# Kernel optimization log

Hardware: AMD Instinct MI355X
Metric: run time of the kernel (lower is better)

## Reference

```python
import math
import jax, jax.numpy as jnp
import numpy as np

SR = 48000
FRAME_HOP = 240
F0_MIN = 20.0
F0_MAX = 5000.0
F0_BINS = 64
VEL_DIM = 8
N_HARM = 128
NOISE_FFT = 1024
N_NOISE = NOISE_FFT // 2 + 1
HOP = NOISE_FFT // 4
PAD = NOISE_FFT // 2


def lin_interp(x, size):
    # matches F.interpolate(mode='linear', align_corners=False) along last axis
    T_in = x.shape[-1]
    pos = (jnp.arange(size, dtype=jnp.float32) + 0.5) * (T_in / size) - 0.5
    pos = jnp.clip(pos, 0.0, T_in - 1.0)
    lo = jnp.floor(pos).astype(jnp.int32)
    hi = jnp.minimum(lo + 1, T_in - 1)
    fr = pos - lo.astype(jnp.float32)
    return x[..., lo] * (1.0 - fr) + x[..., hi] * fr


def encode_f0(f0):
    f0s = jnp.clip(f0, F0_MIN, None)
    fn = jnp.clip((jnp.log(f0s) - math.log(F0_MIN)) / (math.log(F0_MAX) - math.log(F0_MIN)), 0.0, 1.0)
    i = jnp.arange(1, F0_BINS // 2 + 1, dtype=jnp.float32)
    ang = math.pi * i * fn[..., None]  # (B,T,bins/2)
    enc = jnp.stack([jnp.sin(ang), jnp.cos(ang)], axis=-1).reshape(f0.shape + (F0_BINS,))
    return enc * (f0 > 0).astype(jnp.float32)[..., None]


def encode_velocity(vel):
    vn = jnp.clip(vel.astype(jnp.float32) / 7.0, 0.0, 1.0)
    i = jnp.arange(1, VEL_DIM // 2 + 1, dtype=jnp.float32)
    ang = math.pi * i * vn[..., None]
    return jnp.stack([jnp.sin(ang), jnp.cos(ang)], axis=-1).reshape(vel.shape + (VEL_DIM,))


def gru(x, W_ih, W_hh, b_ih, b_hh):
    # torch nn.GRU, 1 layer, batch_first; gate order r,z,n
    B, T, _ = x.shape
    H = W_hh.shape[1]
    gi = x @ W_ih.T + b_ih  # (B,T,3H)

    def step(h, g):
        gh = h @ W_hh.T + b_hh
        ir, iz, in_ = jnp.split(g, 3, axis=-1)
        hr, hz, hn = jnp.split(gh, 3, axis=-1)
        r = jax.nn.sigmoid(ir + hr)
        z = jax.nn.sigmoid(iz + hz)
        n = jnp.tanh(in_ + r * hn)
        h = (1.0 - z) * n + z * h
        return h, h

    _, hs = jax.lax.scan(step, jnp.zeros((B, H), x.dtype), jnp.swapaxes(gi, 0, 1))
    return jnp.swapaxes(hs, 0, 1)


def harmonic_synth(harm_amps, f0_hz, n_samples, inh):
    # harm_amps (B,T,N), f0_hz (B,T), inh (B,) -> (B,S)
    B, T, N = harm_amps.shape
    a = lin_interp(jnp.transpose(harm_amps, (0, 2, 1)), n_samples)        # (B,N,S)
    f0_up = lin_interp(f0_hz[:, None, :], n_samples)[:, 0]               # (B,S)
    k = jnp.arange(1, N + 1, dtype=jnp.float32)
    stretch = jnp.sqrt(1.0 + inh[:, None] * k ** 2)                      # (B,N)
    inst_freq = f0_up[:, None, :] * (k[None, :] * stretch)[:, :, None]   # (B,N,S)
    mask = (inst_freq < SR * 0.45).astype(a.dtype)
    f0_mean = f0_up.mean(axis=-1)
    n_active = jnp.maximum((k[None, :] * f0_mean[:, None] < SR * 0.45).sum(axis=1), 1).astype(a.dtype)
    phase = jnp.cumsum(2.0 * jnp.pi * inst_freq / SR, axis=-1)
    sig = (a * mask * jnp.sin(phase)).sum(axis=1)
    return sig / n_active[:, None]


def noise_synth(noise_mags, f0_hz, n_samples, noise):
    # noise_mags (B,T,513), noise (B,S) -> (B,S)
    B, T, N = noise_mags.shape
    window = 0.5 - 0.5 * jnp.cos(2.0 * jnp.pi * jnp.arange(NOISE_FFT, dtype=jnp.float32) / NOISE_FFT)  # hann, periodic
    padded = jnp.pad(noise, ((0, 0), (PAD, PAD)), mode='reflect')
    T_stft = 1 + n_samples // HOP
    idx = jnp.arange(T_stft)[:, None] * HOP + jnp.arange(NOISE_FFT)[None, :]  # (T_stft, n_fft)
    frames = padded[:, idx] * window                                          # (B,T_stft,n_fft)
    spec = jnp.fft.rfft(frames)                                               # (B,T_stft,513)
    mag_up = lin_interp(jnp.transpose(noise_mags, (0, 2, 1)), T_stft)         # (B,513,T_stft)
    f0_mean = jnp.clip(f0_hz, F0_MIN, None).mean(axis=1)                      # (B,)
    freqs = jnp.arange(N_NOISE, dtype=jnp.float32) * (SR / NOISE_FFT)
    src = jnp.clip(freqs[None, :] / f0_mean[:, None] * (N / N_HARM), 0.0, N - 1.0)  # (B,513)
    lo = src.astype(jnp.int32)
    hi = jnp.minimum(lo + 1, N - 1)
    fr = (src - lo.astype(jnp.float32))[:, :, None]
    lo_e = jnp.broadcast_to(lo[:, :, None], (B, N_NOISE, T_stft))
    hi_e = jnp.broadcast_to(hi[:, :, None], (B, N_NOISE, T_stft))
    v_lo = jnp.take_along_axis(mag_up, lo_e, axis=1)
    v_hi = jnp.take_along_axis(mag_up, hi_e, axis=1)
    mag_abs = v_lo + fr * (v_hi - v_lo)                                       # (B,513,T_stft)
    shaped = spec * jnp.transpose(mag_abs, (0, 2, 1))                         # (B,T_stft,513)
    tframes = jnp.fft.irfft(shaped, n=NOISE_FFT) * window                     # (B,T_stft,n_fft)
    Lp = NOISE_FFT + (T_stft - 1) * HOP
    flat = idx.reshape(-1)
    ola = jnp.zeros((B, Lp), jnp.float32).at[:, flat].add(tframes.reshape(B, -1))
    wsq = jnp.zeros((Lp,), jnp.float32).at[flat].add(jnp.tile(window ** 2, T_stft))
    out = ola / jnp.where(wsq > 1e-11, wsq, 1.0)
    return out[:, PAD:PAD + n_samples]


def ddsp_forward(f0_hz, loudness_db, noise_L, noise_R,
                 W_pre1, b_pre1, W_pre2, b_pre2, W_ih, W_hh, b_ih, b_hh,
                 W_post, b_post, W_harm, b_harm, W_amp, b_amp,
                 W_noise, b_noise, W_namp, b_namp, W_B, b_B, velocity):
    B, T = f0_hz.shape
    n_samples = T * FRAME_HOP
    feat = jnp.concatenate([encode_f0(f0_hz),
                            jnp.broadcast_to(encode_velocity(velocity)[:, None, :], (B, T, VEL_DIM))], axis=-1)
    feat = jax.nn.relu(feat @ W_pre1 + b_pre1)
    feat = jax.nn.relu(feat @ W_pre2 + b_pre2)
    feat = gru(feat, W_ih, W_hh, b_ih, b_hh)
    feat = jax.nn.relu(feat @ W_post + b_post)
    # stereo heads stacked on channel axis c in {L,R}
    harm_dist = jax.nn.softmax(jnp.einsum('btd,cdn->cbtn', feat, W_harm) + b_harm[:, None, None, :], axis=-1)
    harm_amp = jax.nn.softplus(jnp.einsum('btd,cd->cbt', feat, W_amp) + b_amp[:, None, None])
    harm_amps = harm_dist * harm_amp[..., None]                               # (2,B,T,128)
    nmag = jax.nn.sigmoid(jnp.einsum('btd,cdn->cbtn', feat, W_noise) + b_noise[:, None, None, :])
    nmag = nmag * jax.nn.softplus(jnp.einsum('btd,cd->cbt', feat, W_namp) + b_namp[:, None, None])[..., None]
    f0_mean = jnp.clip(f0_hz, F0_MIN, None).mean(axis=1)
    midi = 69.0 + 12.0 * jnp.log2(f0_mean / 440.0)
    b_max = 0.0008 * jnp.exp(-(midi - 21.0) / 88.0 * math.log(10.0))
    inh = jax.nn.sigmoid(feat @ W_B + b_B[0]).mean(axis=1) * b_max           # inh_scale = 1.0
    hL = harmonic_synth(harm_amps[0], f0_hz, n_samples, inh)
    hR = harmonic_synth(harm_amps[1], f0_hz, n_samples, inh)
    nL = noise_synth(nmag[0], f0_hz, n_samples, noise_L)
    nR = noise_synth(nmag[1], f0_hz, n_samples, noise_R)
    lo_up = lin_interp((10.0 ** (loudness_db / 20.0))[:, None, :], n_samples)[:, 0]
    return jnp.stack([(hL + nL) * lo_up, (hR + nR) * lo_up], axis=1)         # (B,2,S)


def setup_inputs() -> dict:
    key = jax.random.key(0)
    ks = iter(jax.random.split(key, 40))
    B, T = 2, 400
    S = T * FRAME_HOP
    rnd = lambda shape, s=0.05: jax.random.normal(next(ks), shape, jnp.float32) * s
    d = {}
    d['f0_hz'] = 100.0 + 400.0 * jax.random.uniform(next(ks), (B, T), jnp.float32)
    d['loudness_db'] = -30.0 + 5.0 * jax.random.normal(next(ks), (B, T), jnp.float32)
    d['noise_L'] = jax.random.normal(next(ks), (B, S), jnp.float32)
    d['noise_R'] = jax.random.normal(next(ks), (B, S), jnp.float32)
    d['W_pre1'] = rnd((72, 128)); d['b_pre1'] = rnd((128,))
    d['W_pre2'] = rnd((128, 128)); d['b_pre2'] = rnd((128,))
    d['W_ih'] = rnd((192, 128)); d['W_hh'] = rnd((192, 64))
    d['b_ih'] = rnd((192,)); d['b_hh'] = rnd((192,))
    d['W_post'] = rnd((64, 128)); d['b_post'] = rnd((128,))
    d['W_harm'] = rnd((2, 128, N_HARM)); d['b_harm'] = rnd((2, N_HARM))
    d['W_amp'] = rnd((2, 128)); d['b_amp'] = rnd((2,))
    d['W_noise'] = rnd((2, 128, N_NOISE)); d['b_noise'] = rnd((2, N_NOISE)) - 3.0
    d['W_namp'] = rnd((2, 128)); d['b_namp'] = rnd((2,)) - 3.0
    d['W_B'] = rnd((128,)); d['b_B'] = rnd((1,)) - 5.0
    d['velocity'] = jax.random.randint(next(ks), (B,), 0, 8, dtype=jnp.int32)
    return d


def reference(f0_hz, loudness_db, noise_L, noise_R,
              W_pre1, b_pre1, W_pre2, b_pre2, W_ih, W_hh, b_ih, b_hh,
              W_post, b_post, W_harm, b_harm, W_amp, b_amp,
              W_noise, b_noise, W_namp, b_namp, W_B, b_B, velocity):
    return ddsp_forward(f0_hz, loudness_db, noise_L, noise_R,
                        W_pre1, b_pre1, W_pre2, b_pre2, W_ih, W_hh, b_ih, b_hh,
                        W_post, b_post, W_harm, b_harm, W_amp, b_amp,
                        W_noise, b_noise, W_namp, b_namp, W_B, b_B, velocity)
```

## Files before the change

### kernel.cpp

```cpp
#include <hip/hip_runtime.h>
#include <math.h>

#define Tn   400
#define Bn   2
#define Sn   96000
#define NHh  128
#define NNn  513
#define NFFT 1024
#define HOPs 256
#define PADs 512
#define TS   376
#define LPn  97024
#define CUT  21600.0f
#define DPI  3.14159265358979323846

__device__ __forceinline__ float sigmoidf_(float x){ return 1.0f/(1.0f+expf(-x)); }
__device__ __forceinline__ float softplusf_(float x){ return fmaxf(x,0.0f)+log1pf(expf(-fabsf(x))); }
__device__ __forceinline__ float fsigmoid_(float x){ return __fdividef(1.0f, 1.0f + __expf(-x)); }
__device__ __forceinline__ float ftanh_(float x){
  float e = __expf(fminf(fmaxf(2.0f*x, -30.0f), 30.0f));
  return __fdividef(e - 1.0f, e + 1.0f);
}

__global__ void k_setup(const float* f0, float* fs, double* P) {
  int b = threadIdx.x;
  if (b < Bn) {
    const float* f = f0 + b*Tn;
    double sm = 0.0;
    for (int t=0;t<Tn;t++) sm += fmax((double)f[t], 20.0);
    float f0m = (float)(sm / (double)Tn);
    fs[b] = f0m;
    float midi = 69.0f + 12.0f * log2f(f0m/440.0f);
    fs[2+b] = 0.0008f * expf(-(midi-21.0f)*(1.0f/88.0f) * 2.302585093f);
    double* Pb = P + b*Tn;
    double acc = 0.0;
    for (int m=0;m<Tn;m++){ Pb[m] = acc; if (m < Tn-1) acc += (double)f[m] + (double)f[m+1]; }
    double Ctot = 120.0*((double)f[0] + Pb[Tn-1] + (double)f[Tn-1]);
    double fupmean = Ctot / (double)Sn;
    int cnt = 0;
    for (int k=1;k<=NHh;k++) if ((float)k * (float)fupmean < CUT) cnt++;
    if (cnt < 1) cnt = 1;
    fs[4+b] = (float)cnt;
  }
}

__global__ void __launch_bounds__(128) k_frame1(
    const float* f0, const int* vel,
    const float* Wp1, const float* bp1,
    const float* Wp2, const float* bp2,
    const float* Wih, const float* bih,
    float* gi) {
  int bt = blockIdx.x; int b = bt / Tn, t = bt % Tn;
  __shared__ float x[72];
  __shared__ float y1[128];
  __shared__ float y2[128];
  int tid = threadIdx.x;
  if (tid < 72) {
    if (tid < 64) {
      float fv = f0[b*Tn+t];
      float fsv = fmaxf(fv, 20.0f);
      float fn = (logf(fsv) - 2.99573227355399f) * (1.0f/5.52146091786225f);
      fn = fminf(fmaxf(fn,0.0f),1.0f);
      int j = (tid>>1) + 1;
      float ang = (float)DPI * (float)j * fn;
      x[tid] = (tid & 1) ? cosf(ang) : sinf(ang);
    } else {
      int i = tid - 64;
      float vn = fminf(fmaxf((float)vel[b]*(1.0f/7.0f),0.0f),1.0f);
      int j = (i>>1)+1;
      float ang = (float)DPI * (float)j * vn;
      x[tid] = (i & 1) ? cosf(ang) : sinf(ang);
    }
  }
  __syncthreads();
  {
    float a = bp1[tid];
    #pragma unroll 8
    for (int i=0;i<72;i++) a += x[i]*Wp1[i*128+tid];
    y1[tid] = fmaxf(a,0.0f);
  }
  __syncthreads();
  {
    float a = bp2[tid];
    #pragma unroll 8
    for (int i=0;i<128;i++) a += y1[i]*Wp2[i*128+tid];
    y2[tid] = fmaxf(a,0.0f);
  }
  __syncthreads();
  float* gout = gi + ((size_t)b*Tn + t)*192;
  for (int g = tid; g < 192; g += 128) {
    float s = bih[g];
    const float* wr = Wih + g*128;
    #pragma unroll 8
    for (int d=0; d<128; d++) s += y2[d]*wr[d];
    gout[g] = s;
  }
}

#define MV4(wv, xv) { a0=fmaf((wv).x,(xv).x,a0); a1=fmaf((wv).y,(xv).y,a1); \
                      a2=fmaf((wv).z,(xv).z,a2); a3=fmaf((wv).w,(xv).w,a3); }

__global__ void __launch_bounds__(256, 1) k_gru(const float* __restrict__ gi,
                                                const float* __restrict__ Whh,
                                                const float* __restrict__ bhh,
                                                float* __restrict__ hsout) {
  int b = blockIdx.x;
  int j = threadIdx.x;
  __shared__ float h[64];
  __shared__ float s[192];
  const float* gib = gi + (size_t)b*Tn*192;
  float* hb_ = hsout + (size_t)b*Tn*64;

  float4 w0,w1,w2,w3,w4,w5,w6,w7,w8,w9,w10,w11,w12,w13,w14,w15;
  float bj = 0.0f;
  if (j < 192) {
    const float4* W4 = (const float4*)(Whh + (size_t)j*64);
    w0=W4[0];  w1=W4[1];  w2=W4[2];   w3=W4[3];
    w4=W4[4];  w5=W4[5];  w6=W4[6];   w7=W4[7];
    w8=W4[8];  w9=W4[9];  w10=W4[10]; w11=W4[11];
    w12=W4[12];w13=W4[13];w14=W4[14]; w15=W4[15];
    bj = bhh[j];
    if (j < 64) h[j] = 0.0f;
  }
  int u = j - 192;
  float hu = 0.0f;
  float ga[8], gz_[8], gn_[8], hist[8];
  if (j >= 192) {
    #pragma unroll
    for (int i=0;i<8;i++) {
      ga[i]  = gib[(size_t)i*192 + u];
      gz_[i] = gib[(size_t)i*192 + 64 + u];
      gn_[i] = gib[(size_t)i*192 + 128 + u];
    }
  }
  __syncthreads();

  for (int c=0;c<50;c++) {
    #pragma unroll
    for (int i=0;i<8;i++) {
      if (j < 192) {
        const float4* h4 = (const float4*)h;
        float4 x0=h4[0], x1=h4[1], x2=h4[2],  x3=h4[3];
        float4 x4=h4[4], x5=h4[5], x6=h4[6],  x7=h4[7];
        float4 x8=h4[8], x9=h4[9], x10=h4[10],x11=h4[11];
        float4 x12=h4[12],x13=h4[13],x14=h4[14],x15=h4[15];
        float a0=bj, a1=0.f, a2=0.f, a3=0.f;
        MV4(w0,x0)   MV4(w1,x1)   MV4(w2,x2)   MV4(w3,x3)
        MV4(w4,x4)   MV4(w5,x5)   MV4(w6,x6)   MV4(w7,x7)
        MV4(w8,x8)   MV4(w9,x9)   MV4(w10,x10) MV4(w11,x11)
        MV4(w12,x12) MV4(w13,x13) MV4(w14,x14) MV4(w15,x15)
        s[j] = ((a0+a1)+(a2+a3));
      }
      __syncthreads();
      if (j >= 192) {
        float mr = s[u], mz = s[64+u], mn = s[128+u];
        float rg = fsigmoid_(ga[i]  + mr);
        float zg = fsigmoid_(gz_[i] + mz);
        float ng = ftanh_(gn_[i] + rg*mn);
        hu = (1.0f - zg)*ng + zg*hu;
        h[u] = hu;
        hist[i] = hu;
      }
      __syncthreads();
    }
    if (j >= 192) {
      int t0 = c*8;
      #pragma unroll
      for (int i=0;i<8;i++) hb_[(size_t)(t0+i)*64 + u] = hist[i];
      if (c < 49) {
        int t1 = t0 + 8;
        #pragma unroll
        for (int i=0;i<8;i++) {
          ga[i]  = gib[(size_t)(t1+i)*192 + u];
          gz_[i] = gib[(size_t)(t1+i)*192 + 64 + u];
          gn_[i] = gib[(size_t)(t1+i)*192 + 128 + u];
        }
      }
    }
  }
}

__global__ void __launch_bounds__(256) k_heads(
    const float* hs, const float* Wpost, const float* bpost,
    const float* Wharm, const float* bharm,
    const float* Wamp, const float* bamp,
    const float* Wnoise, const float* bnoise,
    const float* Wnamp, const float* bnamp,
    const float* WB, const float* bB,
    float* harm, float* nmag, float* fs) {
  int bt = blockIdx.x; int b = bt / Tn, t = bt % Tn;
  __shared__ float h64[64];
  __shared__ float fp[128];
  __shared__ float lg[256];
  __shared__ float red[8];
  int tid = threadIdx.x;
  if (tid < 64) h64[tid] = hs[((size_t)b*Tn+t)*64+tid];
  __syncthreads();
  if (tid < 128) {
    float a = bpost[tid];
    #pragma unroll 8
    for (int i=0;i<64;i++) a += h64[i]*Wpost[i*128+tid];
    fp[tid] = fmaxf(a,0.0f);
  }
  __syncthreads();
  {
    int c = tid >> 7, n = tid & 127;
    float a = bharm[c*128+n];
    const float* w = Wharm + (size_t)c*128*128 + n;
    #pragma unroll 8
    for (int d=0;d<128;d++) a += fp[d]*w[d*128];
    lg[tid] = a;
  }
  __syncthreads();
  if (tid < 2) {
    const float* l = lg + tid*128;
    float mx = l[0];
    for (int n=1;n<128;n++) mx = fmaxf(mx,l[n]);
    float sm = 0.f; for (int n=0;n<128;n++) sm += expf(l[n]-mx);
    red[tid] = mx; red[2+tid] = sm;
    float aa = bamp[tid];
    for (int d=0;d<128;d++) aa += fp[d]*Wamp[tid*128+d];
    red[4+tid] = softplusf_(aa);
    float na = bnamp[tid];
    for (int d=0;d<128;d++) na += fp[d]*Wnamp[tid*128+d];
    red[6+tid] = softplusf_(na);
  } else if (tid == 2) {
    float bb = bB[0];
    for (int d=0;d<128;d++) bb += fp[d]*WB[d];
    atomicAdd(&fs[6+b], sigmoidf_(bb));
  }
  __syncthreads();
  {
    int c = tid >> 7, n = tid & 127;
    float v = expf(lg[tid]-red[c]) / red[2+c] * red[4+c];
    harm[(((size_t)c*Bn + b)*Tn + t)*128 + n] = v;
  }
  for (int o = tid; o < 2*NNn; o += 256) {
    int c = (o < NNn) ? 0 : 1; int n = o - c*NNn;
    float a = bnoise[c*NNn+n];
    const float* w = Wnoise + (size_t)c*128*NNn + n;
    #pragma unroll 8
    for (int d=0;d<128;d++) a += fp[d]*w[(size_t)d*NNn];
    nmag[(((size_t)c*Bn + b)*Tn + t)*NNn + n] = sigmoidf_(a) * red[6+c];
  }
}

__global__ void k_inh(float* fs, double* rk) {
  int tid = threadIdx.x;
  __shared__ double inh_s[2];
  if (tid < 2) {
    float inh = fs[6+tid]*(1.0f/(float)Tn) * fs[2+tid];
    fs[8+tid] = inh;
    inh_s[tid] = (double)inh;
  }
  __syncthreads();
  int b = tid >> 7, k = (tid & 127) + 1;
  double kk = (double)k;
  rk[b*128 + (k-1)] = kk * sqrt(1.0 + inh_s[b]*kk*kk);
}

__global__ void __launch_bounds__(256) k_harm(
    const float* f0, const float* harm, const double* P,
    const double* rk, const float* fs, float* sigh) {
  int b = blockIdx.y;
  int s = blockIdx.x*256 + threadIdx.x;
  __shared__ double rks[128];
  __shared__ float  rkf[128];
  if (threadIdx.x < 128) {
    double r = rk[b*128+threadIdx.x];
    rks[threadIdx.x] = r; rkf[threadIdx.x] = (float)r;
  }
  __syncthreads();
  const float* f = f0 + b*Tn;
  float posf = ((float)s + 0.5f) * (400.0f/96000.0f) - 0.5f;
  posf = fminf(fmaxf(posf, 0.0f), 399.0f);
  int lo = (int)floorf(posf);
  int hi = min(lo+1, 399);
  float fr = posf - (float)lo;
  float f0up = f[lo]*(1.0f-fr) + f[hi]*fr;
  double C;
  if (s < 120) {
    C = (double)(s+1) * (double)f[0];
  } else if (s < 95880) {
    int m = (s-120)/240;
    int j = s - 120 - 240*m;
    double fm = (double)f[m], fm1 = (double)f[m+1];
    double jp = (double)(j+1);
    C = 120.0*((double)f[0] + P[b*Tn+m]) + jp*fm + (fm1-fm)*jp*jp*(1.0/480.0);
  } else {
    C = 120.0*((double)f[0] + P[b*Tn+399]) + (double)(s-95880+1)*(double)f[399];
  }
  double Phi = C * (2.0*DPI/48000.0);
  const float* hLlo = harm + (((size_t)0*Bn + b)*Tn + lo)*128;
  const float* hLhi = harm + (((size_t)0*Bn + b)*Tn + hi)*128;
  const float* hRlo = harm + (((size_t)1*Bn + b)*Tn + lo)*128;
  const float* hRhi = harm + (((size_t)1*Bn + b)*Tn + hi)*128;
  float accL=0.f, accR=0.f;
  for (int k=0;k<128;k++) {
    float finst = f0up * rkf[k];
    if (finst < CUT) {
      double u = rks[k]*Phi * (1.0/(2.0*DPI));
      u -= floor(u);
      float sv = __sinf((float)u * 6.28318530717959f);
      float aL = hLlo[k]*(1.0f-fr) + hLhi[k]*fr;
      float aR = hRlo[k]*(1.0f-fr) + hRhi[k]*fr;
      accL += aL*sv; accR += aR*sv;
    }
  }
  float na = fs[4+b];
  sigh[((size_t)b*2+0)*Sn + s] = accL/na;
  sigh[((size_t)b*2+1)*Sn + s] = accR/na;
}

__global__ void __launch_bounds__(256) k_noise(
    const float* noiseL, const float* noiseR,
    const float* nmag, const float* fs, float* ola) {
  int t = blockIdx.x;
  int sig = blockIdx.y;
  int b = sig >> 1, c = sig & 1;
  const float* noise = (c==0 ? noiseL : noiseR) + (size_t)b*Sn;
  __shared__ float re[1024], im[1024];
  __shared__ float twc[512], tws[512];
  __shared__ float wdw[1024];
  int tid = threadIdx.x;
  for (int j=tid; j<512; j+=256) {
    float ang = (float)(2.0*DPI) * (float)j * (1.0f/1024.0f);
    twc[j] = cosf(ang); tws[j] = sinf(ang);
  }
  for (int i=tid; i<1024; i+=256)
    wdw[i] = 0.5f - 0.5f*cosf((float)(2.0*DPI)*(float)i*(1.0f/1024.0f));
  __syncthreads();
  for (int i=tid;i<1024;i+=256) {
    int q = t*HOPs + i - PADs;
    if (q < 0) q = -q;
    if (q >= Sn) q = 2*Sn - 2 - q;
    float v = noise[q]*wdw[i];
    int br = (int)(__brev((unsigned)i) >> 22);
    re[br] = v; im[br] = 0.0f;
  }
  __syncthreads();
  for (int st=1; st<=10; st++) {
    int half = 1<<(st-1);
    #pragma unroll
    for (int w=0;w<2;w++) {
      int bid = tid + w*256;
      int pos = bid & (half-1);
      int i0 = ((bid >> (st-1)) << st) + pos;
      int i1 = i0 + half;
      int j = pos << (10-st);
      float cr = twc[j], ci = -tws[j];
      float xr = re[i1], xi = im[i1];
      float tr = cr*xr - ci*xi, ti = cr*xi + ci*xr;
      float ar = re[i0], ai = im[i0];
      re[i1] = ar - tr; im[i1] = ai - ti;
      re[i0] = ar + tr; im[i0] = ai + ti;
    }
    __syncthreads();
  }
  float f0m = fs[b];
  float pp = ((float)t + 0.5f) * (400.0f/376.0f) - 0.5f;
  pp = fminf(fmaxf(pp,0.0f),399.0f);
  int tlo = (int)floorf(pp); int thi = min(tlo+1, 399); float tfr = pp - (float)tlo;
  const float* nm = nmag + (((size_t)c*Bn + b)*Tn)*NNn;
  for (int k=tid;k<=512;k+=256) {
    float src = (float)k * 46.875f / f0m * (513.0f/128.0f);
    src = fminf(fmaxf(src,0.0f),512.0f);
    int flo = (int)src; int fhi = min(flo+1,512); float ffr = src - (float)flo;
    float vlo = nm[(size_t)tlo*NNn+flo]*(1.0f-tfr) + nm[(size_t)thi*NNn+flo]*tfr;
    float vhi = nm[(size_t)tlo*NNn+fhi]*(1.0f-tfr) + nm[(size_t)thi*NNn+fhi]*tfr;
    float mag = vlo + ffr*(vhi-vlo);
    re[k] *= mag; im[k] *= mag;
  }
  __syncthreads();
  for (int k=tid+513; k<1024; k+=256) {
    re[k] = re[1024-k]; im[k] = -im[1024-k];
  }
  __syncthreads();
  for (int i=tid;i<1024;i+=256) {
    int j = (int)(__brev((unsigned)i)>>22);
    if (i < j) {
      float a=re[i]; re[i]=re[j]; re[j]=a;
      float bb=im[i]; im[i]=im[j]; im[j]=bb;
    }
  }
  __syncthreads();
  for (int st=1; st<=10; st++) {
    int half = 1<<(st-1);
    #pragma unroll
    for (int w=0;w<2;w++) {
      int bid = tid + w*256;
      int pos = bid & (half-1);
      int i0 = ((bid >> (st-1)) << st) + pos;
      int i1 = i0 + half;
      int j = pos << (10-st);
      float cr = twc[j], ci = tws[j];
      float xr = re[i1], xi = im[i1];
      float tr = cr*xr - ci*xi, ti = cr*xi + ci*xr;
      float ar = re[i0], ai = im[i0];
      re[i1] = ar - tr; im[i1] = ai - ti;
      re[i0] = ar + tr; im[i0] = ai + ti;
    }
    __syncthreads();
  }
  float* olab = ola + (size_t)sig*LPn;
  for (int i=tid;i<1024;i+=256) {
    float y = re[i] * (1.0f/1024.0f) * wdw[i];
    atomicAdd(&olab[t*HOPs + i], y);
  }
}

__global__ void __launch_bounds__(256) k_final(
    const float* loud, const float* sigh, const float* ola, float* out) {
  int b = blockIdx.y;
  int s = blockIdx.x*256 + threadIdx.x;
  float posf = ((float)s + 0.5f)*(400.0f/96000.0f) - 0.5f;
  posf = fminf(fmaxf(posf,0.0f),399.0f);
  int lo=(int)floorf(posf); int hi=min(lo+1,399); float fr=posf-(float)lo;
  const float* ld = loud + b*Tn;
  float lv = exp10f(ld[lo]*0.05f)*(1.0f-fr) + exp10f(ld[hi]*0.05f)*fr;
  int p = PADs + s;
  int t0 = (p >= 1023) ? ((p - 1023 + 255) >> 8) : 0;
  int t1 = min(TS-1, p >> 8);
  float wsq = 0.0f;
  for (int t=t0;t<=t1;t++) {
    int i = p - (t<<8);
    float w = 0.5f - 0.5f*cosf((float)(2.0*DPI)*(float)i*(1.0f/1024.0f));
    wsq += w*w;
  }
  float denom = (wsq > 1e-11f) ? wsq : 1.0f;
  for (int c=0;c<2;c++) {
    float hv = sigh[((size_t)b*2+c)*Sn+s];
    float nv = ola[(size_t)(b*2+c)*LPn + p] / denom;
    out[((size_t)b*2+c)*Sn + s] = (hv + nv)*lv;
  }
}

extern "C" void kernel_launch(void* const* d_in, const int* in_sizes, int n_in,
                              void* d_out, int out_size, void* d_ws, size_t ws_size,
                              hipStream_t stream) {
  const float* f0    = (const float*)d_in[0];
  const float* loud  = (const float*)d_in[1];
  const float* nL    = (const float*)d_in[2];
  const float* nR    = (const float*)d_in[3];
  const float* Wp1   = (const float*)d_in[4];  const float* bp1 = (const float*)d_in[5];
  const float* Wp2   = (const float*)d_in[6];  const float* bp2 = (const float*)d_in[7];
  const float* Wih   = (const float*)d_in[8];  const float* Whh = (const float*)d_in[9];
  const float* bih   = (const float*)d_in[10]; const float* bhh = (const float*)d_in[11];
  const float* Wpost = (const float*)d_in[12]; const float* bpost=(const float*)d_in[13];
  const float* Wharm = (const float*)d_in[14]; const float* bharm=(const float*)d_in[15];
  const float* Wamp  = (const float*)d_in[16]; const float* bamp =(const float*)d_in[17];
  const float* Wnoise= (const float*)d_in[18]; const float* bnoise=(const float*)d_in[19];
  const float* Wnamp = (const float*)d_in[20]; const float* bnamp=(const float*)d_in[21];
  const float* WB    = (const float*)d_in[22]; const float* bB  = (const float*)d_in[23];
  const int*   vel   = (const int*)d_in[24];
  float* out = (float*)d_out;

  char* w = (char*)d_ws;
  double* P    = (double*)w; w += (size_t)Bn*Tn*sizeof(double);
  double* rk   = (double*)w; w += (size_t)Bn*128*sizeof(double);
  float* gi    = (float*)w;  w += (size_t)Bn*Tn*192*sizeof(float);
  float* hsb   = (float*)w;  w += (size_t)Bn*Tn*64*sizeof(float);
  float* harm  = (float*)w;  w += (size_t)2*Bn*Tn*128*sizeof(float);
  float* nmag  = (float*)w;  w += (size_t)2*Bn*Tn*NNn*sizeof(float);
  float* sigh  = (float*)w;  w += (size_t)Bn*2*Sn*sizeof(float);
  float* ola   = (float*)w;  w += (size_t)Bn*2*LPn*sizeof(float);
  float* fscal = (float*)w;  w += 32*sizeof(float);

  hipMemsetAsync(ola, 0, (size_t)Bn*2*LPn*sizeof(float) + 32*sizeof(float), stream);

  k_setup<<<1, 64, 0, stream>>>(f0, fscal, P);
  k_frame1<<<Bn*Tn, 128, 0, stream>>>(f0, vel, Wp1,bp1, Wp2,bp2, Wih,bih, gi);
  k_gru<<<Bn, 256, 0, stream>>>(gi, Whh, bhh, hsb);
  k_heads<<<Bn*Tn, 256, 0, stream>>>(hsb, Wpost,bpost, Wharm,bharm, Wamp,bamp,
                                     Wnoise,bnoise, Wnamp,bnamp, WB,bB,
                                     harm, nmag, fscal);
  k_inh<<<1, 256, 0, stream>>>(fscal, rk);
  dim3 gh(Sn/256, Bn);
  k_harm<<<gh, 256, 0, stream>>>(f0, harm, P, rk, fscal, sigh);
  dim3 gn(TS, Bn*2);
  k_noise<<<gn, 256, 0, stream>>>(nL, nR, nmag, fscal, ola);
  dim3 gf(Sn/256, Bn);
  k_final<<<gf, 256, 0, stream>>>(loud, sigh, ola, out);
}
```

Measured before the change: 464.0 us.

## Overlap forward noise FFT with GRU scan and split GRU matvec across waves

The forward STFT of the input noise does not depend on the network, so it now runs in extra blocks of the GRU kernel. Those blocks fill idle CUs while the two serial GRU blocks scan, and the spectra go to a workspace buffer that a new noise kernel reads for only the filter and inverse FFT. The GRU matvec is also split four ways over 768 threads, each holding a quarter row of weights, with a partial-sum reduction in the gate threads. This adds spectrum traffic and an 832-thread launch, and falls back to the old path if the workspace is too small.

After: 425.6 us. 1.09x faster.

```diff
diff --git a/kernel.cpp b/kernel.cpp
--- a/kernel.cpp
+++ b/kernel.cpp
@@ -97,35 +97,81 @@
   }
 }
 
-#define MV4(wv, xv) { a0=fmaf((wv).x,(xv).x,a0); a1=fmaf((wv).y,(xv).y,a1); \
-                      a2=fmaf((wv).z,(xv).z,a2); a3=fmaf((wv).w,(xv).w,a3); }
-
-__global__ void __launch_bounds__(256, 1) k_gru(const float* __restrict__ gi,
-                                                const float* __restrict__ Whh,
-                                                const float* __restrict__ bhh,
-                                                float* __restrict__ hsout) {
+__global__ void __launch_bounds__(832, 1) k_grufft(
+    const float* __restrict__ gi, const float* __restrict__ Whh,
+    const float* __restrict__ bhh, float* __restrict__ hsout,
+    const float* __restrict__ noiseL, const float* __restrict__ noiseR,
+    float2* __restrict__ spec) {
+  __shared__ float h[64];
+  __shared__ float sp[768];
+  __shared__ float re[1024], im[1024];
+  __shared__ float twc[512], tws[512];
+  __shared__ float wdw[1024];
+  int j = threadIdx.x;
+
+  if (blockIdx.x >= 2) {
+    if (j >= 256) return;
+    int idx = blockIdx.x - 2;
+    int sig = idx / TS, t = idx % TS;
+    int b = sig >> 1, c = sig & 1;
+    const float* noise = (c==0 ? noiseL : noiseR) + (size_t)b*Sn;
+    int tid = j;
+    for (int q=tid; q<512; q+=256) {
+      float ang = (float)(2.0*DPI) * (float)q * (1.0f/1024.0f);
+      twc[q] = cosf(ang); tws[q] = sinf(ang);
+    }
+    for (int i=tid; i<1024; i+=256)
+      wdw[i] = 0.5f - 0.5f*cosf((float)(2.0*DPI)*(float)i*(1.0f/1024.0f));
+    __syncthreads();
+    for (int i=tid;i<1024;i+=256) {
+      int q = t*HOPs + i - PADs;
+      if (q < 0) q = -q;
+      if (q >= Sn) q = 2*Sn - 2 - q;
+      float v = noise[q]*wdw[i];
+      int br = (int)(__brev((unsigned)i) >> 22);
+      re[br] = v; im[br] = 0.0f;
+    }
+    __syncthreads();
+    for (int st=1; st<=10; st++) {
+      int half = 1<<(st-1);
+      #pragma unroll
+      for (int w=0;w<2;w++) {
+        int bid = tid + w*256;
+        int pos = bid & (half-1);
+        int i0 = ((bid >> (st-1)) << st) + pos;
+        int i1 = i0 + half;
+        int q = pos << (10-st);
+        float cr = twc[q], ci = -tws[q];
+        float xr = re[i1], xi = im[i1];
+        float tr = cr*xr - ci*xi, ti = cr*xi + ci*xr;
+        float ar = re[i0], ai = im[i0];
+        re[i1] = ar - tr; im[i1] = ai - ti;
+        re[i0] = ar + tr; im[i0] = ai + ti;
+      }
+      __syncthreads();
+    }
+    float2* so = spec + ((size_t)sig*TS + t)*NNn;
+    for (int k=tid;k<=512;k+=256) so[k] = make_float2(re[k], im[k]);
+    return;
+  }
+
   int b = blockIdx.x;
-  int j = threadIdx.x;
-  __shared__ float h[64];
-  __shared__ float s[192];
   const float* gib = gi + (size_t)b*Tn*192;
   float* hb_ = hsout + (size_t)b*Tn*64;
-
-  float4 w0,w1,w2,w3,w4,w5,w6,w7,w8,w9,w10,w11,w12,w13,w14,w15;
-  float bj = 0.0f;
-  if (j < 192) {
-    const float4* W4 = (const float4*)(Whh + (size_t)j*64);
-    w0=W4[0];  w1=W4[1];  w2=W4[2];   w3=W4[3];
-    w4=W4[4];  w5=W4[5];  w6=W4[6];   w7=W4[7];
-    w8=W4[8];  w9=W4[9];  w10=W4[10]; w11=W4[11];
-    w12=W4[12];w13=W4[13];w14=W4[14]; w15=W4[15];
-    bj = bhh[j];
+  int wv = j >> 6, lane = j & 63;
+  int p = wv / 3;
+  int row = (wv % 3)*64 + lane;
+  float4 w0,w1,w2,w3;
+  if (j < 768) {
+    const float4* W4 = (const float4*)(Whh + (size_t)row*64 + p*16);
+    w0=W4[0]; w1=W4[1]; w2=W4[2]; w3=W4[3];
     if (j < 64) h[j] = 0.0f;
   }
-  int u = j - 192;
-  float hu = 0.0f;
+  int u = lane;
+  float hu = 0.0f, br=0.f, bz=0.f, bn=0.f;
   float ga[8], gz_[8], gn_[8], hist[8];
-  if (j >= 192) {
+  if (j >= 768) {
+    br = bhh[u]; bz = bhh[64+u]; bn = bhh[128+u];
     #pragma unroll
     for (int i=0;i<8;i++) {
       ga[i]  = gib[(size_t)i*192 + u];
@@ -138,32 +184,34 @@
   for (int c=0;c<50;c++) {
     #pragma unroll
     for (int i=0;i<8;i++) {
-      if (j < 192) {
+      if (j < 768) {
         const float4* h4 = (const float4*)h;
-        float4 x0=h4[0], x1=h4[1], x2=h4[2],  x3=h4[3];
-        float4 x4=h4[4], x5=h4[5], x6=h4[6],  x7=h4[7];
-        float4 x8=h4[8], x9=h4[9], x10=h4[10],x11=h4[11];
-        float4 x12=h4[12],x13=h4[13],x14=h4[14],x15=h4[15];
-        float a0=bj, a1=0.f, a2=0.f, a3=0.f;
-        MV4(w0,x0)   MV4(w1,x1)   MV4(w2,x2)   MV4(w3,x3)
-        MV4(w4,x4)   MV4(w5,x5)   MV4(w6,x6)   MV4(w7,x7)
-        MV4(w8,x8)   MV4(w9,x9)   MV4(w10,x10) MV4(w11,x11)
-        MV4(w12,x12) MV4(w13,x13) MV4(w14,x14) MV4(w15,x15)
-        s[j] = ((a0+a1)+(a2+a3));
+        float4 x0=h4[p*4+0], x1=h4[p*4+1], x2=h4[p*4+2], x3=h4[p*4+3];
+        float a0,a1,a2,a3;
+        a0 = w0.x*x0.x; a1 = w0.y*x0.y; a2 = w0.z*x0.z; a3 = w0.w*x0.w;
+        a0 = fmaf(w1.x,x1.x,a0); a1 = fmaf(w1.y,x1.y,a1);
+        a2 = fmaf(w1.z,x1.z,a2); a3 = fmaf(w1.w,x1.w,a3);
+        a0 = fmaf(w2.x,x2.x,a0); a1 = fmaf(w2.y,x2.y,a1);
+        a2 = fmaf(w2.z,x2.z,a2); a3 = fmaf(w2.w,x2.w,a3);
+        a0 = fmaf(w3.x,x3.x,a0); a1 = fmaf(w3.y,x3.y,a1);
+        a2 = fmaf(w3.z,x3.z,a2); a3 = fmaf(w3.w,x3.w,a3);
+        sp[p*192 + row] = (a0+a1)+(a2+a3);
       }
       __syncthreads();
-      if (j >= 192) {
-        float mr = s[u], mz = s[64+u], mn = s[128+u];
-        float rg = fsigmoid_(ga[i]  + mr);
-        float zg = fsigmoid_(gz_[i] + mz);
-        float ng = ftanh_(gn_[i] + rg*mn);
+      if (j >= 768) {
+        float mr = (sp[u]      + sp[192+u])     + (sp[384+u]     + sp[576+u]);
+        float mz = (sp[64+u]   + sp[192+64+u])  + (sp[384+64+u]  + sp[576+64+u]);
+        float mn = (sp[128+u]  + sp[192+128+u]) + (sp[384+128+u] + sp[576+128+u]);
+        float rg = fsigmoid_(ga[i]  + br + mr);
+        float zg = fsigmoid_(gz_[i] + bz + mz);
+        float ng = ftanh_(gn_[i] + rg*(bn + mn));
         hu = (1.0f - zg)*ng + zg*hu;
         h[u] = hu;
         hist[i] = hu;
       }
       __syncthreads();
     }
-    if (j >= 192) {
+    if (j >= 768) {
       int t0 = c*8;
       #pragma unroll
       for (int i=0;i<8;i++) hb_[(size_t)(t0+i)*64 + u] = hist[i];
@@ -312,7 +360,77 @@
   sigh[((size_t)b*2+1)*Sn + s] = accR/na;
 }
 
-__global__ void __launch_bounds__(256) k_noise(
+__global__ void __launch_bounds__(256) k_noise2(
+    const float2* __restrict__ spec,
+    const float* nmag, const float* fs, float* ola) {
+  int t = blockIdx.x;
+  int sig = blockIdx.y;
+  int b = sig >> 1, c = sig & 1;
+  __shared__ float re[1024], im[1024];
+  __shared__ float twc[512], tws[512];
+  __shared__ float wdw[1024];
+  int tid = threadIdx.x;
+  for (int q=tid; q<512; q+=256) {
+    float ang = (float)(2.0*DPI) * (float)q * (1.0f/1024.0f);
+    twc[q] = cosf(ang); tws[q] = sinf(ang);
+  }
+  for (int i=tid; i<1024; i+=256)
+    wdw[i] = 0.5f - 0.5f*cosf((float)(2.0*DPI)*(float)i*(1.0f/1024.0f));
+  float f0m = fs[b];
+  float pp = ((float)t + 0.5f) * (400.0f/376.0f) - 0.5f;
+  pp = fminf(fmaxf(pp,0.0f),399.0f);
+  int tlo = (int)floorf(pp); int thi = min(tlo+1, 399); float tfr = pp - (float)tlo;
+  const float* nm = nmag + (((size_t)c*Bn + b)*Tn)*NNn;
+  const float2* so = spec + ((size_t)sig*TS + t)*NNn;
+  for (int k=tid;k<=512;k+=256) {
+    float src = (float)k * 46.875f / f0m * (513.0f/128.0f);
+    src = fminf(fmaxf(src,0.0f),512.0f);
+    int flo = (int)src; int fhi = min(flo+1,512); float ffr = src - (float)flo;
+    float vlo = nm[(size_t)tlo*NNn+flo]*(1.0f-tfr) + nm[(size_t)thi*NNn+flo]*tfr;
+    float vhi = nm[(size_t)tlo*NNn+fhi]*(1.0f-tfr) + nm[(size_t)thi*NNn+fhi]*tfr;
+    float mag = vlo + ffr*(vhi-vlo);
+    float2 v = so[k];
+    re[k] = v.x*mag; im[k] = v.y*mag;
+  }
+  __syncthreads();
+  for (int k=tid+513; k<1024; k+=256) {
+    re[k] = re[1024-k]; im[k] = -im[1024-k];
+  }
+  __syncthreads();
+  for (int i=tid;i<1024;i+=256) {
+    int jx = (int)(__brev((unsigned)i)>>22);
+    if (i < jx) {
+      float a=re[i]; re[i]=re[jx]; re[jx]=a;
+      float bb=im[i]; im[i]=im[jx]; im[jx]=bb;
+    }
+  }
+  __syncthreads();
+  for (int st=1; st<=10; st++) {
+    int half = 1<<(st-1);
+    #pragma unroll
+    for (int w=0;w<2;w++) {
+      int bid = tid + w*256;
+      int pos = bid & (half-1);
+      int i0 = ((bid >> (st-1)) << st) + pos;
+      int i1 = i0 + half;
+      int q = pos << (10-st);
+      float cr = twc[q], ci = tws[q];
+      float xr = re[i1], xi = im[i1];
+      float tr = cr*xr - ci*xi, ti = cr*xi + ci*xr;
+      float ar = re[i0], ai = im[i0];
+      re[i1] = ar - tr; im[i1] = ai - ti;
+      re[i0] = ar + tr; im[i0] = ai + ti;
+    }
+    __syncthreads();
+  }
+  float* olab = ola + (size_t)sig*LPn;
+  for (int i=tid;i<1024;i+=256) {
+    float y = re[i] * (1.0f/1024.0f) * wdw[i];
+    atomicAdd(&olab[t*HOPs + i], y);
+  }
+}
+
+__global__ void __launch_bounds__(256) k_noiseB(
     const float* noiseL, const float* noiseR,
     const float* nmag, const float* fs, float* ola) {
   int t = blockIdx.x;
@@ -323,9 +441,9 @@
   __shared__ float twc[512], tws[512];
   __shared__ float wdw[1024];
   int tid = threadIdx.x;
-  for (int j=tid; j<512; j+=256) {
-    float ang = (float)(2.0*DPI) * (float)j * (1.0f/1024.0f);
-    twc[j] = cosf(ang); tws[j] = sinf(ang);
+  for (int q=tid; q<512; q+=256) {
+    float ang = (float)(2.0*DPI) * (float)q * (1.0f/1024.0f);
+    twc[q] = cosf(ang); tws[q] = sinf(ang);
   }
   for (int i=tid; i<1024; i+=256)
     wdw[i] = 0.5f - 0.5f*cosf((float)(2.0*DPI)*(float)i*(1.0f/1024.0f));
@@ -347,8 +465,8 @@
       int pos = bid & (half-1);
       int i0 = ((bid >> (st-1)) << st) + pos;
       int i1 = i0 + half;
-      int j = pos << (10-st);
-      float cr = twc[j], ci = -tws[j];
+      int q = pos << (10-st);
+      float cr = twc[q], ci = -tws[q];
       float xr = re[i1], xi = im[i1];
       float tr = cr*xr - ci*xi, ti = cr*xi + ci*xr;
       float ar = re[i0], ai = im[i0];
@@ -377,10 +495,10 @@
   }
   __syncthreads();
   for (int i=tid;i<1024;i+=256) {
-    int j = (int)(__brev((unsigned)i)>>22);
-    if (i < j) {
-      float a=re[i]; re[i]=re[j]; re[j]=a;
-      float bb=im[i]; im[i]=im[j]; im[j]=bb;
+    int jx = (int)(__brev((unsigned)i)>>22);
+    if (i < jx) {
+      float a=re[i]; re[i]=re[jx]; re[jx]=a;
+      float bb=im[i]; im[i]=im[jx]; im[jx]=bb;
     }
   }
   __syncthreads();
@@ -392,8 +510,8 @@
       int pos = bid & (half-1);
       int i0 = ((bid >> (st-1)) << st) + pos;
       int i1 = i0 + half;
-      int j = pos << (10-st);
-      float cr = twc[j], ci = tws[j];
+      int q = pos << (10-st);
+      float cr = twc[q], ci = tws[q];
       float xr = re[i1], xi = im[i1];
       float tr = cr*xr - ci*xi, ti = cr*xi + ci*xr;
       float ar = re[i0], ai = im[i0];
@@ -465,12 +583,18 @@
   float* sigh  = (float*)w;  w += (size_t)Bn*2*Sn*sizeof(float);
   float* ola   = (float*)w;  w += (size_t)Bn*2*LPn*sizeof(float);
   float* fscal = (float*)w;  w += 32*sizeof(float);
+  float2* spec = (float2*)w; w += (size_t)4*TS*NNn*sizeof(float2);
+  bool fused = ((size_t)(w - (char*)d_ws) <= ws_size);
 
   hipMemsetAsync(ola, 0, (size_t)Bn*2*LPn*sizeof(float) + 32*sizeof(float), stream);
 
   k_setup<<<1, 64, 0, stream>>>(f0, fscal, P);
   k_frame1<<<Bn*Tn, 128, 0, stream>>>(f0, vel, Wp1,bp1, Wp2,bp2, Wih,bih, gi);
-  k_gru<<<Bn, 256, 0, stream>>>(gi, Whh, bhh, hsb);
+  if (fused) {
+    k_grufft<<<2 + 4*TS, 832, 0, stream>>>(gi, Whh, bhh, hsb, nL, nR, spec);
+  } else {
+    k_grufft<<<2, 832, 0, stream>>>(gi, Whh, bhh, hsb, nL, nR, (float2*)ola);
+  }
   k_heads<<<Bn*Tn, 256, 0, stream>>>(hsb, Wpost,bpost, Wharm,bharm, Wamp,bamp,
                                      Wnoise,bnoise, Wnamp,bnamp, WB,bB,
                                      harm, nmag, fscal);
@@ -478,7 +602,11 @@
   dim3 gh(Sn/256, Bn);
   k_harm<<<gh, 256, 0, stream>>>(f0, harm, P, rk, fscal, sigh);
   dim3 gn(TS, Bn*2);
-  k_noise<<<gn, 256, 0, stream>>>(nL, nR, nmag, fscal, ola);
+  if (fused) {
+    k_noise2<<<gn, 256, 0, stream>>>(spec, nmag, fscal, ola);
+  } else {
+    k_noiseB<<<gn, 256, 0, stream>>>(nL, nR, nmag, fscal, ola);
+  }
   dim3 gf(Sn/256, Bn);
   k_final<<<gf, 256, 0, stream>>>(loud, sigh, ola, out);
 }
```
